# Performance work log

Measured on AMD Instinct MI355X. Metric: run time of the kernel, lower is better.

## Reference

```python
import jax, jax.numpy as jnp
from jax import lax
import numpy as np

BLANK = 0
PAD = 1
LABEL_SMOOTHING = 0.1
CE_SCALE = 1.0
TEMPERATURE = 1.0

B, T, U1, D, V = 8, 128, 33, 512, 4096  # U1 = U + 1


def setup_inputs() -> dict:
    key = jax.random.key(0)
    k0, k1, k2, k3, k4 = jax.random.split(key, 5)
    x = jax.random.normal(k0, (B, T, U1, D), dtype=jnp.float32)
    weight = jax.random.normal(k1, (V, D), dtype=jnp.float32) * 0.02
    bias = jnp.zeros((V,), dtype=jnp.float32)
    src_lengths = jax.random.randint(k2, (B,), T // 2, T + 1, dtype=jnp.int32)
    tgt_lengths = jax.random.randint(k3, (B,), U1 // 2, U1, dtype=jnp.int32)
    targets = jax.random.randint(k4, (B, U1 - 1), 2, V, dtype=jnp.int32)
    pos = jnp.arange(U1 - 1, dtype=jnp.int32)
    targets = jnp.where(pos[None, :] < tgt_lengths[:, None], targets, PAD)
    return {'x': x, 'weight': weight, 'bias': bias, 'targets': targets,
            'src_lengths': src_lengths, 'tgt_lengths': tgt_lengths}


def _rnnt_neglogp(blank_lp, emit_lp, src_lengths, tgt_lengths):
    """RNN-T forward DP. blank_lp: (B,T,U1) log P(blank); emit_lp: (B,T,U) log P(y_u).
    Returns per-utterance negative log-likelihood, shape (B,)."""
    Bn, Tn, U1n = blank_lp.shape
    # alpha at t=0: can only emit labels -> prefix-sum of emit log-probs
    alpha0 = jnp.concatenate(
        [jnp.zeros((Bn, 1), blank_lp.dtype), jnp.cumsum(emit_lp[:, 0, :], axis=1)], axis=1)

    def t_step(alpha_prev, xs):
        blank_prev, emit_t = xs  # (B,U1), (B,U)
        a = alpha_prev + blank_prev  # blank transition from t-1
        def u_step(c, xu):
            a_u, e_prev = xu  # each (B,)
            c = jnp.logaddexp(a_u, c + e_prev)  # emit transition from u-1 at same t
            return c, c
        _, rest = lax.scan(u_step, a[:, 0], (a[:, 1:].T, emit_t.T))  # rest: (U,B)
        alpha_t = jnp.concatenate([a[:, :1], rest.T], axis=1)
        return alpha_t, alpha_t

    xs = (jnp.swapaxes(blank_lp[:, :-1], 0, 1), jnp.swapaxes(emit_lp[:, 1:], 0, 1))
    _, alphas_rest = lax.scan(t_step, alpha0, xs)  # (T-1,B,U1)
    alphas = jnp.concatenate([alpha0[None], alphas_rest], axis=0)  # (T,B,U1)
    bidx = jnp.arange(Bn)
    alpha_last_t = alphas[src_lengths - 1, bidx]  # (B,U1)
    a_fin = jnp.take_along_axis(alpha_last_t, tgt_lengths[:, None], axis=1)[:, 0]
    b_fin = blank_lp[bidx, src_lengths - 1, tgt_lengths]  # final blank emission
    return -(a_fin + b_fin)


def reference(x, weight, bias, targets, src_lengths, tgt_lengths):
    Vn = weight.shape[0]
    # joint logits over full lattice: (B,T,U1,V)
    logits = (jnp.einsum('btud,vd->btuv', x, weight) + bias).astype(jnp.float32)
    lp = jax.nn.log_softmax(logits / TEMPERATURE, axis=-1)
    blank_lp = lp[..., BLANK]  # (B,T,U1)
    emit_lp = jnp.take_along_axis(lp[:, :, :-1, :], targets[:, None, :, None].astype(jnp.int32), axis=3)[..., 0]  # (B,T,U)
    loss_prob = jnp.sum(_rnnt_neglogp(blank_lp, emit_lp, src_lengths, tgt_lengths))
    loss_delay = jnp.zeros((), jnp.float32)  # delay_func == 'zero'
    # label-smoothed CE on last valid encoder frame
    last_h = jnp.take_along_axis(x, (src_lengths - 1)[:, None, None, None], axis=1)[:, 0]  # (B,U1,D)
    last_h = last_h[:, :-1]  # (B,U,D)
    ce_logits = (jnp.einsum('bud,vd->buv', last_h, weight) + bias).astype(jnp.float32)
    lprobs = jax.nn.log_softmax(ce_logits, axis=-1)
    nll = -jnp.take_along_axis(lprobs, targets[..., None], axis=-1)[..., 0]  # (B,U)
    smooth = -jnp.sum(lprobs, axis=-1)
    mask = (targets != PAD).astype(lprobs.dtype)
    eps_i = LABEL_SMOOTHING / (Vn - 1)
    loss_smoothed = jnp.sum(((1.0 - LABEL_SMOOTHING - eps_i) * nll + eps_i * smooth) * mask)
    total = loss_prob + loss_delay + CE_SCALE * loss_smoothed
    return total
```

## Files before the change

### kernel.cpp

```cpp
#include <hip/hip_runtime.h>
#include <hip/hip_bf16.h>
#include <math.h>
#include <stdint.h>

#define B_ 8
#define T_ 128
#define U1_ 33
#define D_ 512
#define V_ 4096
#define M_ (B_*T_*U1_)

#define BLANK_ 0
#define PAD_ 1

#define TM 128
#define TN 128
#define BKB 128
#define NK (D_/BKB)
#define GN (V_/TN)

typedef __attribute__((ext_vector_type(4))) float fvec4;
typedef __attribute__((ext_vector_type(8))) int   i8v;
typedef __attribute__((ext_vector_type(4))) int   i4v;

#define SCALE_A 0x7F7F7F7Fu
#define SCALE_B 0x79797979u

__device__ __forceinline__ void load_lds16(const uint8_t* g, uint8_t* l) {
    __builtin_amdgcn_global_load_lds(
        (const __attribute__((address_space(1))) unsigned int*)g,
        (__attribute__((address_space(3))) unsigned int*)l, 16, 0, 0);
}

__device__ __forceinline__ unsigned pack4_fp8(fvec4 v) {
    int r = __builtin_amdgcn_cvt_pk_fp8_f32(v.x, v.y, 0, false);
    r = __builtin_amdgcn_cvt_pk_fp8_f32(v.z, v.w, r, true);
    return (unsigned)r;
}

__global__ void convert_kernel(const float* __restrict__ x, const float* __restrict__ w,
                               const float* __restrict__ bias,
                               uint8_t* __restrict__ xf8, uint8_t* __restrict__ wf8,
                               float* __restrict__ wsum)
{
    int i = blockIdx.x * 256 + threadIdx.x;
    int stride = gridDim.x * 256;
    const int nx = (M_ * D_) / 16;
    const int nw = (V_ * D_) / 16;
    for (int j = i; j < nx; j += stride) {
        const fvec4* p = (const fvec4*)x + (size_t)j * 4;
        uint4 o = { pack4_fp8(p[0]), pack4_fp8(p[1]), pack4_fp8(p[2]), pack4_fp8(p[3]) };
        ((uint4*)xf8)[j] = o;
    }
    for (int j = i; j < nw; j += stride) {
        const fvec4* p = (const fvec4*)w + (size_t)j * 4;
        fvec4 v0 = p[0]*64.0f, v1 = p[1]*64.0f, v2 = p[2]*64.0f, v3 = p[3]*64.0f;
        uint4 o = { pack4_fp8(v0), pack4_fp8(v1), pack4_fp8(v2), pack4_fp8(v3) };
        ((uint4*)wf8)[j] = o;
    }
    if (blockIdx.x < 32) {
        const int t = threadIdx.x;
        const int v0 = blockIdx.x * 128;
        float s0 = 0.0f, s1 = 0.0f;
        for (int v = 0; v < 128; v++) {
            s0 += w[(size_t)(v0 + v) * D_ + t];
            s1 += w[(size_t)(v0 + v) * D_ + t + 256];
        }
        atomicAdd(&wsum[t], s0);
        atomicAdd(&wsum[t + 256], s1);
        if (blockIdx.x == 0) {
            float bsum = 0.0f;
            for (int v = t; v < V_; v += 256) bsum += bias[v];
            atomicAdd(&wsum[D_], bsum);
        }
    }
}

__global__ __launch_bounds__(256, 2)
void gemm_fused(const uint8_t* __restrict__ xf8, const uint8_t* __restrict__ wf8,
                const float* __restrict__ bias, const int* __restrict__ targets,
                float* __restrict__ partial_e,
                float* __restrict__ blank_z, float* __restrict__ emit_z)
{
    __shared__ __align__(16) uint8_t As[2][TM * BKB];
    __shared__ __align__(16) uint8_t Bs[2][TN * BKB];
    __shared__ float ps[TM];
    __shared__ int tgt_s[TM];

    const int tid  = threadIdx.x;
    const int lane = tid & 63;
    const int wid  = tid >> 6;

    const int fid = blockIdx.y * gridDim.x + blockIdx.x;
    const int xcd = fid & 7;
    const int idx = fid >> 3;
    const int mt  = xcd * 33 + (idx >> 5);
    const int nt  = idx & 31;
    const int m0  = mt * TM;
    const int n0  = nt * TN;

    const int srow = wid * 32 + (lane >> 3);
    const int schk = (lane & 7) ^ ((lane >> 3) & 7);
    const uint8_t* agp = xf8 + (size_t)(m0 + srow) * D_ + schk * 16;
    const uint8_t* bgp = wf8 + (size_t)(n0 + srow) * D_ + schk * 16;

    fvec4 acc[4][4];
#pragma unroll
    for (int i = 0; i < 4; i++)
#pragma unroll
        for (int j = 0; j < 4; j++) acc[i][j] = (fvec4)0.0f;

    const int wrow = (wid >> 1) * 64;
    const int wcol = (wid & 1) * 64;
    const int m15  = lane & 15;
    const int quad = lane >> 4;

    auto stage = [&](int buf, int ks) {
        const uint8_t* ag = agp + ks * BKB;
        const uint8_t* bg = bgp + ks * BKB;
#pragma unroll
        for (int j = 0; j < 4; j++) {
            load_lds16(ag + j * 8 * D_, &As[buf][(wid * 32 + j * 8) * BKB]);
            load_lds16(bg + j * 8 * D_, &Bs[buf][(wid * 32 + j * 8) * BKB]);
        }
    };

    stage(0, 0);
    __syncthreads();

    const int e   = m15 & 7;
    const int c0b = (((quad << 1) ^ e) << 4);

    for (int ks = 0; ks < NK; ks++) {
        const int cur = ks & 1;
        if (ks + 1 < NK) stage(cur ^ 1, ks + 1);

        i8v fa[4], fb[4];
#pragma unroll
        for (int mi = 0; mi < 4; mi++) {
            int base = (wrow + mi * 16 + m15) << 7;
            union { i4v h[2]; i8v w; } u;
            u.h[0] = *(const i4v*)&As[cur][base + c0b];
            u.h[1] = *(const i4v*)&As[cur][base + (c0b ^ 16)];
            fa[mi] = u.w;
        }
#pragma unroll
        for (int ni = 0; ni < 4; ni++) {
            int base = (wcol + ni * 16 + m15) << 7;
            union { i4v h[2]; i8v w; } u;
            u.h[0] = *(const i4v*)&Bs[cur][base + c0b];
            u.h[1] = *(const i4v*)&Bs[cur][base + (c0b ^ 16)];
            fb[ni] = u.w;
        }
#pragma unroll
        for (int mi = 0; mi < 4; mi++)
#pragma unroll
            for (int ni = 0; ni < 4; ni++)
                acc[mi][ni] = __builtin_amdgcn_mfma_scale_f32_16x16x128_f8f6f4(
                                  fa[mi], fb[ni], acc[mi][ni],
                                  0, 0,
                                  0, SCALE_A, 0, SCALE_B);
        __syncthreads();
    }

    if (tid < TM) {
        ps[tid] = 0.0f;
        int row = m0 + tid;
        int u = row % U1_;
        int b = row / (T_ * U1_);
        tgt_s[tid] = (u < U1_ - 1) ? targets[b * (U1_ - 1) + u] : -1;
    }
    __syncthreads();

    float bv[4];
#pragma unroll
    for (int ni = 0; ni < 4; ni++) bv[ni] = bias[n0 + wcol + ni * 16 + m15];

    const bool blank_lane = (nt == 0) && (wcol == 0) && (m15 == 0);

#pragma unroll
    for (int mi = 0; mi < 4; mi++) {
#pragma unroll
        for (int r = 0; r < 4; r++) {
            const int irow = wrow + mi * 16 + quad * 4 + r;
            float se = 0.0f;
#pragma unroll
            for (int ni = 0; ni < 4; ni++) {
                float z = acc[mi][ni][r] + bv[ni];
                se += __expf(z);
                int c = n0 + wcol + ni * 16 + m15;
                if (tgt_s[irow] == c) emit_z[m0 + irow] = z;
            }
            if (blank_lane) blank_z[m0 + irow] = acc[mi][0][r] + bv[0];
            se += __shfl_xor(se, 1, 64);
            se += __shfl_xor(se, 2, 64);
            se += __shfl_xor(se, 4, 64);
            se += __shfl_xor(se, 8, 64);
            if (m15 == 0) atomicAdd(&ps[irow], se);
        }
    }
    __syncthreads();
    if (tid < TM) {
        partial_e[(size_t)nt * M_ + m0 + tid] = ps[tid];
    }
}

__global__ __launch_bounds__(256)
void dp_kernel(const float* __restrict__ partial_e,
               const float* __restrict__ blank_z, const float* __restrict__ emit_z,
               const int* __restrict__ targets,
               const int* __restrict__ src_lengths, const int* __restrict__ tgt_lengths,
               const float* __restrict__ x, const float* __restrict__ wsum,
               float* __restrict__ out)
{
    __shared__ float blp[T_ * U1_];
    __shared__ float elp[T_ * U1_];
    const int tid = threadIdx.x;
    const int b = blockIdx.x;
    const int sl = src_lengths[b], tl = tgt_lengths[b];

    for (int i = tid; i < T_ * U1_; i += 256) {
        int g = b * T_ * U1_ + i;
        float se = 0.0f;
#pragma unroll
        for (int j = 0; j < GN; j++) se += partial_e[(size_t)j * M_ + g];
        float l = __logf(se);
        blp[i] = blank_z[g] - l;
        elp[i] = emit_z[g] - l;
    }
    __syncthreads();

    if (tid >= 64) {
        if (tid < 64 + (U1_ - 1)) {
            int u = tid - 64;
            int tgt = targets[b * (U1_ - 1) + u];
            if (tgt != PAD_) {
                int i = (sl - 1) * U1_ + u;
                int g = b * T_ * U1_ + i;
                float se = 0.0f;
#pragma unroll
                for (int j = 0; j < GN; j++) se += partial_e[(size_t)j * M_ + g];
                float l = __logf(se);
                float sz = wsum[D_];
                const fvec4* xr = (const fvec4*)(x + (size_t)g * D_);
                const fvec4* ws = (const fvec4*)wsum;
#pragma unroll 4
                for (int d = 0; d < D_ / 4; d++) {
                    fvec4 a = xr[d], wv = ws[d];
                    sz += a.x * wv.x + a.y * wv.y + a.z * wv.z + a.w * wv.w;
                }
                float nll    = l - emit_z[g];
                float smooth = (float)V_ * l - sz;
                const float eps_i = 0.1f / (float)(V_ - 1);
                atomicAdd(out, (1.0f - 0.1f - eps_i) * nll + eps_i * smooth);
            }
        }
        return;
    }

    const int u = tid;
    const int ua = (u < U1_) ? u : U1_ - 1;

    float val = 0.0f;
    float afin = 0.0f;

    for (int d = 1; d <= (T_ - 1) + (U1_ - 1); d++) {
        int t = d - u;
        int tb = t - 1; tb = tb < 0 ? 0 : (tb > T_ - 1 ? T_ - 1 : tb);
        int tc = t < 0 ? 0 : (t > T_ - 1 ? T_ - 1 : t);
        float blv = blp[tb * U1_ + ua];
        float elv = elp[tc * U1_ + (ua > 0 ? ua - 1 : 0)];
        float up = __shfl_up(val, 1, 64);
        bool valid = (u < U1_) && (t >= 0) && (t < T_);
        if (valid) {
            if (t == 0) {
                val = up + elv;
            } else if (u == 0) {
                val = val + blv;
            } else {
                float a1 = val + blv;
                float a2 = up + elv;
                float mx = fmaxf(a1, a2), mn = fminf(a1, a2);
                val = mx + log1pf(__expf(mn - mx));
            }
            if (t == sl - 1 && u == tl) afin = val;
        }
    }
#pragma unroll
    for (int off = 1; off < 64; off <<= 1) afin += __shfl_xor(afin, off, 64);
    if (u == 0) {
        float bfin = blp[(sl - 1) * U1_ + tl];
        atomicAdd(out, -(afin + bfin));
    }
}

extern "C" void kernel_launch(void* const* d_in, const int* in_sizes, int n_in,
                              void* d_out, int out_size, void* d_ws, size_t ws_size,
                              hipStream_t stream)
{
    const float* x           = (const float*)d_in[0];
    const float* w           = (const float*)d_in[1];
    const float* bias        = (const float*)d_in[2];
    const int*   targets     = (const int*)d_in[3];
    const int*   src_lengths = (const int*)d_in[4];
    const int*   tgt_lengths = (const int*)d_in[5];
    float* out = (float*)d_out;

    char* p = (char*)d_ws;
    uint8_t* xf8 = (uint8_t*)p;     p += (size_t)M_ * D_;
    uint8_t* wf8 = (uint8_t*)p;     p += (size_t)V_ * D_;
    float* partial_e = (float*)p;   p += (size_t)GN * M_ * sizeof(float);
    float* blank_z   = (float*)p;   p += (size_t)M_ * sizeof(float);
    float* emit_z    = (float*)p;   p += (size_t)M_ * sizeof(float);
    float* wsum      = (float*)p;   p += (size_t)(D_ + 4) * sizeof(float);

    hipMemsetAsync(out, 0, sizeof(float), stream);
    hipMemsetAsync(wsum, 0, (D_ + 4) * sizeof(float), stream);

    convert_kernel<<<1536, 256, 0, stream>>>(x, w, bias, xf8, wf8, wsum);
    gemm_fused<<<dim3(M_/TM, V_/TN), 256, 0, stream>>>(xf8, wf8, bias, targets,
                                                       partial_e, blank_z, emit_z);
    dp_kernel<<<B_, 256, 0, stream>>>(partial_e, blank_z, emit_z, targets,
                                      src_lengths, tgt_lengths, x, wsum, out);
}
```

Measured before the change: 418.6 us.

## Reduce log-sum-exp partials in last-arriving GEMM tile instead of DP kernel

Each GEMM block bumps a per-row-tile atomic counter after writing its partial exp sums. The last block to finish a row tile sums all column partials and writes the final log-sum-exp. The DP kernel, which runs as only 8 blocks, then reads one value per row instead of reducing 32 partials, moving that serial reduction into the wide GEMM grid. The cost is a threadfence and an atomic per GEMM block, plus a counter array that must be zeroed with the existing memset.

```diff
diff --git a/kernel.cpp b/kernel.cpp
--- a/kernel.cpp
+++ b/kernel.cpp
@@ -18,6 +18,7 @@
 #define BKB 128
 #define NK (D_/BKB)
 #define GN (V_/TN)
+#define NMT (M_/TM)
 
 typedef __attribute__((ext_vector_type(4))) float fvec4;
 typedef __attribute__((ext_vector_type(8))) int   i8v;
@@ -79,13 +80,15 @@
 __global__ __launch_bounds__(256, 2)
 void gemm_fused(const uint8_t* __restrict__ xf8, const uint8_t* __restrict__ wf8,
                 const float* __restrict__ bias, const int* __restrict__ targets,
-                float* __restrict__ partial_e,
+                float* __restrict__ partial_e, float* __restrict__ lse,
+                int* __restrict__ tilecnt,
                 float* __restrict__ blank_z, float* __restrict__ emit_z)
 {
     __shared__ __align__(16) uint8_t As[2][TM * BKB];
     __shared__ __align__(16) uint8_t Bs[2][TN * BKB];
     __shared__ float ps[TM];
     __shared__ int tgt_s[TM];
+    __shared__ int lastdone;
 
     const int tid  = threadIdx.x;
     const int lane = tid & 63;
@@ -203,10 +206,24 @@
     if (tid < TM) {
         partial_e[(size_t)nt * M_ + m0 + tid] = ps[tid];
     }
+
+    __threadfence();
+    if (tid == 0) {
+        int c = atomicAdd(&tilecnt[mt], 1);
+        lastdone = (c == GN - 1);
+    }
+    __syncthreads();
+    if (lastdone && tid < TM) {
+        int r = m0 + tid;
+        float se = 0.0f;
+#pragma unroll
+        for (int j = 0; j < GN; j++) se += partial_e[(size_t)j * M_ + r];
+        lse[r] = __logf(se);
+    }
 }
 
 __global__ __launch_bounds__(256)
-void dp_kernel(const float* __restrict__ partial_e,
+void dp_kernel(const float* __restrict__ lse,
                const float* __restrict__ blank_z, const float* __restrict__ emit_z,
                const int* __restrict__ targets,
                const int* __restrict__ src_lengths, const int* __restrict__ tgt_lengths,
@@ -221,10 +238,7 @@
 
     for (int i = tid; i < T_ * U1_; i += 256) {
         int g = b * T_ * U1_ + i;
-        float se = 0.0f;
-#pragma unroll
-        for (int j = 0; j < GN; j++) se += partial_e[(size_t)j * M_ + g];
-        float l = __logf(se);
+        float l = lse[g];
         blp[i] = blank_z[g] - l;
         elp[i] = emit_z[g] - l;
     }
@@ -237,10 +251,7 @@
             if (tgt != PAD_) {
                 int i = (sl - 1) * U1_ + u;
                 int g = b * T_ * U1_ + i;
-                float se = 0.0f;
-#pragma unroll
-                for (int j = 0; j < GN; j++) se += partial_e[(size_t)j * M_ + g];
-                float l = __logf(se);
+                float l = lse[g];
                 float sz = wsum[D_];
                 const fvec4* xr = (const fvec4*)(x + (size_t)g * D_);
                 const fvec4* ws = (const fvec4*)wsum;
@@ -310,16 +321,20 @@
     uint8_t* xf8 = (uint8_t*)p;     p += (size_t)M_ * D_;
     uint8_t* wf8 = (uint8_t*)p;     p += (size_t)V_ * D_;
     float* partial_e = (float*)p;   p += (size_t)GN * M_ * sizeof(float);
+    float* lse       = (float*)p;   p += (size_t)M_ * sizeof(float);
     float* blank_z   = (float*)p;   p += (size_t)M_ * sizeof(float);
     float* emit_z    = (float*)p;   p += (size_t)M_ * sizeof(float);
-    float* wsum      = (float*)p;   p += (size_t)(D_ + 4) * sizeof(float);
+    float* wsum      = (float*)p;
+    int*   tilecnt   = (int*)(p + 516 * sizeof(float));
+    size_t ctrl_bytes = (516 + NMT) * sizeof(int);
 
     hipMemsetAsync(out, 0, sizeof(float), stream);
-    hipMemsetAsync(wsum, 0, (D_ + 4) * sizeof(float), stream);
+    hipMemsetAsync(wsum, 0, ctrl_bytes, stream);
 
     convert_kernel<<<1536, 256, 0, stream>>>(x, w, bias, xf8, wf8, wsum);
     gemm_fused<<<dim3(M_/TM, V_/TN), 256, 0, stream>>>(xf8, wf8, bias, targets,
-                                                       partial_e, blank_z, emit_z);
-    dp_kernel<<<B_, 256, 0, stream>>>(partial_e, blank_z, emit_z, targets,
+                                                       partial_e, lse, tilecnt,
+                                                       blank_z, emit_z);
+    dp_kernel<<<B_, 256, 0, stream>>>(lse, blank_z, emit_z, targets,
                                       src_lengths, tgt_lengths, x, wsum, out);
 }
```

Result: slower. 860.7 us (+105.6%).
